# Kernel optimization log

Measured on AMD Instinct MI355X. Metric: run time of the kernel, lower is better.

## Reference

```python
import jax, jax.numpy as jnp
import numpy as np

N_FEATS = 400000
IN_CH = 64
OUT_CH = 64
KK = 9  # kH * kW for kernel_size=3


def setup_inputs() -> dict:
    key = jax.random.key(0)
    k1, k2, k3, k4 = jax.random.split(key, 4)
    in_feats = jax.random.normal(k1, (N_FEATS, IN_CH), dtype=jnp.float32)
    mask = jnp.ones((N_FEATS,), dtype=bool)
    adj_ids = jax.random.randint(k2, (N_FEATS, KK), 0, N_FEATS, dtype=jnp.int64)
    conv_weight = jax.random.normal(k3, (OUT_CH, KK * IN_CH), dtype=jnp.float32) * 0.02
    conv_bias = jax.random.normal(k4, (OUT_CH,), dtype=jnp.float32) * 0.02
    return {"in_feats": in_feats, "mask": mask, "adj_ids": adj_ids,
            "conv_weight": conv_weight, "conv_bias": conv_bias}


def reference(in_feats, mask, adj_ids, conv_weight, conv_bias):
    # Gather neighbor features: [num_conv_feats, kH*kW, in_channels]
    num_conv_feats = adj_ids.shape[0]
    gathered = in_feats[adj_ids]
    # Flatten kernel window and project: [num_conv_feats, out_channels]
    flat = gathered.reshape(num_conv_feats, -1)
    conv_out = jnp.einsum('nf,of->no', flat, conv_weight) + conv_bias
    # Scatter into masked rows: row i (where mask[i]) receives conv_out row
    # equal to its rank among True mask entries (matches out_feats[mask] = ...).
    pos = jnp.cumsum(mask.astype(jnp.int32)) - 1  # rank among True entries
    pos = jnp.clip(pos, 0, num_conv_feats - 1)
    out_feats = jnp.where(mask[:, None], conv_out[pos], jnp.float32(0))
    return out_feats
```

## Files before the change

kernel.cpp:

```cpp
#include <hip/hip_runtime.h>
#include <hip/hip_bf16.h>


#define KK 9
#define IN_CH 64
#define OUT_CH 64
#define KTOT 576
#define ROWS 16
#define NTILES 25000
#define ROW_BYTES 1152
#define TILE_BYTES 18432
#define NBLK 1024

typedef __attribute__((ext_vector_type(8))) short short8;
typedef __attribute__((ext_vector_type(4))) float f32x4;

__device__ __forceinline__ short bf1(float f) {
  __hip_bfloat16 h = __float2bfloat16(f);
  return *reinterpret_cast<short*>(&h);
}
__device__ __forceinline__ short8 pack8(float4 a, float4 b) {
  short8 v;
  v[0] = bf1(a.x); v[1] = bf1(a.y); v[2] = bf1(a.z); v[3] = bf1(a.w);
  v[4] = bf1(b.x); v[5] = bf1(b.y); v[6] = bf1(b.z); v[7] = bf1(b.w);
  return v;
}

__launch_bounds__(256)
__global__ void prepass_kernel(const float* __restrict__ feats,
                               unsigned short* __restrict__ fb) {
  const size_t idx = (size_t)blockIdx.x * 256 + threadIdx.x;
  const float* p = feats + idx * 8;
  float4 a = *(const float4*)p;
  float4 b = *(const float4*)(p + 4);
  *(short8*)(fb + idx * 8) = pack8(a, b);
}

template <bool PRE>
__launch_bounds__(256, 2)
__global__ void adjconv_kernel(const float* __restrict__ feats,
                               const unsigned short* __restrict__ fb,
                               const unsigned int* __restrict__ adj_raw,
                               const float* __restrict__ W,
                               const float* __restrict__ bias,
                               float* __restrict__ out) {
  __shared__ __align__(16) unsigned char lds[2 * TILE_BYTES];

  const int tid  = threadIdx.x;
  const int lane = tid & 63;
  const int wv   = tid >> 6;
  const int lrow = lane & 15;
  const int kg   = lane >> 4;
  const int bcol = (wv << 4) + lrow;

  bool is64 = true;
  #pragma unroll
  for (int j = 1; j < 16; j += 2) if (adj_raw[j] != 0u) is64 = false;
  const unsigned iscale = is64 ? 2u : 1u;

  short8 bfrag[18];
  #pragma unroll
  for (int ks = 0; ks < 18; ++ks) {
    const float* wp = W + bcol * KTOT + ks * 32 + kg * 8;
    bfrag[ks] = pack8(*(const float4*)wp, *(const float4*)(wp + 4));
  }
  const float bias_c = bias[bcol];

  short8 F[5];
  float4 G[5][2];
  unsigned idn[5];

  auto LOAD_IDS = [&](unsigned* ids, int wt_) {
    const size_t base = (size_t)wt_ * (ROWS * KK);
    #pragma unroll
    for (int i = 0; i < 5; ++i) {
      if (i < 4 || tid < 128) {
        const int cid = tid + (i << 8);
        const int row = cid / 72, ch = cid - row * 72;
        ids[i] = adj_raw[(base + row * KK + (ch >> 3)) * iscale];
      }
    }
  };
  auto GATHER = [&](const unsigned* ids) {
    #pragma unroll
    for (int i = 0; i < 5; ++i) {
      if (i < 4 || tid < 128) {
        const int cid = tid + (i << 8);
        const int row = cid / 72, ch = cid - row * 72;
        const int c8 = (ch & 7) << 3;
        if constexpr (PRE) {
          F[i] = *(const short8*)(fb + (size_t)ids[i] * IN_CH + c8);
        } else {
          const float* p = feats + (size_t)ids[i] * IN_CH + c8;
          G[i][0] = *(const float4*)p;
          G[i][1] = *(const float4*)(p + 4);
        }
      }
    }
  };
  auto WRITE = [&](unsigned char* buf) {
    #pragma unroll
    for (int i = 0; i < 5; ++i) {
      if (i < 4 || tid < 128) {
        const int cid = tid + (i << 8);
        const int row = cid / 72, ch = cid - row * 72;
        unsigned char* dst = buf + row * ROW_BYTES + ((ch ^ (row & 7)) << 4);
        if constexpr (PRE) *(short8*)dst = F[i];
        else               *(short8*)dst = pack8(G[i][0], G[i][1]);
      }
    }
  };

  int wt = blockIdx.x;
  {
    unsigned idc[5];
    LOAD_IDS(idc, wt);
    GATHER(idc);
    if (wt + NBLK < NTILES) LOAD_IDS(idn, wt + NBLK);
    WRITE(lds);
    __syncthreads();
  }

  int cur = 0;
  for (; wt < NTILES; wt += NBLK) {
    const bool hasn1 = (wt + NBLK) < NTILES;
    const bool hasn2 = (wt + 2 * NBLK) < NTILES;
    if (hasn1) GATHER(idn);
    if (hasn2) LOAD_IDS(idn, wt + 2 * NBLK);

    {
      const unsigned char* rbase = lds + cur * TILE_BYTES + lrow * ROW_BYTES;
      f32x4 acc = {0.f, 0.f, 0.f, 0.f};
      #pragma unroll
      for (int ks = 0; ks < 18; ++ks) {
        short8 a = *(const short8*)(rbase + ((((ks << 2) + kg) ^ (lrow & 7)) << 4));
        acc = __builtin_amdgcn_mfma_f32_16x16x32_bf16(a, bfrag[ks], acc, 0, 0, 0);
      }
      float* op = out + ((size_t)wt * ROWS + (kg << 2)) * OUT_CH + bcol;
      op[0 * OUT_CH] = acc[0] + bias_c;
      op[1 * OUT_CH] = acc[1] + bias_c;
      op[2 * OUT_CH] = acc[2] + bias_c;
      op[3 * OUT_CH] = acc[3] + bias_c;
    }

    if (hasn1) WRITE(lds + (cur ^ 1) * TILE_BYTES);
    __syncthreads();
    cur ^= 1;
  }
}

extern "C" void kernel_launch(void* const* d_in, const int* in_sizes, int n_in,
                              void* d_out, int out_size, void* d_ws, size_t ws_size,
                              hipStream_t stream) {
  const float* feats          = (const float*)d_in[0];
  const unsigned int* adj_raw = (const unsigned int*)d_in[2];
  const float* W              = (const float*)d_in[3];
  const float* bias           = (const float*)d_in[4];
  float* out                  = (float*)d_out;

  const size_t FB_BYTES = (size_t)400000 * 64 * 2;

  if (ws_size >= FB_BYTES) {
    unsigned short* fb = (unsigned short*)d_ws;
    hipLaunchKernelGGL(prepass_kernel, dim3(12500), dim3(256), 0, stream, feats, fb);
    hipLaunchKernelGGL((adjconv_kernel<true>), dim3(NBLK), dim3(256), 0, stream,
                       feats, fb, adj_raw, W, bias, out);
  } else {
    hipLaunchKernelGGL((adjconv_kernel<false>), dim3(NBLK), dim3(256), 0, stream,
                       feats, (const unsigned short*)nullptr, adj_raw, W, bias, out);
  }
}
```

Baseline: 123.9 us.

## Gather neighbor rows straight into LDS with global_load_lds and nontemporal I/O

In the bf16 precomputed path, the register-staged gather followed by ds_write is replaced with asynchronous global_load_lds copies of 16 bytes each, straight into the double-buffered LDS tile. The XOR swizzle moves from the LDS address onto the global source column chunk, so each row is stored contiguously while the MFMA reads stay conflict-free. The prepass now uses nontemporal loads and the output uses nontemporal stores. The aim is to cut VGPR pressure and VALU/LDS-write work in the gather stage. It depends on the compiler placing the right vmcnt waits before the barrier for the LDS-DMA writes.

```diff
diff --git a/kernel.cpp b/kernel.cpp
--- a/kernel.cpp
+++ b/kernel.cpp
@@ -14,29 +14,29 @@
 
 typedef __attribute__((ext_vector_type(8))) short short8;
 typedef __attribute__((ext_vector_type(4))) float f32x4;
+typedef float fv4 __attribute__((ext_vector_type(4)));
 
 __device__ __forceinline__ short bf1(float f) {
   __hip_bfloat16 h = __float2bfloat16(f);
   return *reinterpret_cast<short*>(&h);
 }
-__device__ __forceinline__ short8 pack8(float4 a, float4 b) {
+__device__ __forceinline__ short8 pack8(fv4 a, fv4 b) {
   short8 v;
-  v[0] = bf1(a.x); v[1] = bf1(a.y); v[2] = bf1(a.z); v[3] = bf1(a.w);
-  v[4] = bf1(b.x); v[5] = bf1(b.y); v[6] = bf1(b.z); v[7] = bf1(b.w);
+  v[0] = bf1(a[0]); v[1] = bf1(a[1]); v[2] = bf1(a[2]); v[3] = bf1(a[3]);
+  v[4] = bf1(b[0]); v[5] = bf1(b[1]); v[6] = bf1(b[2]); v[7] = bf1(b[3]);
   return v;
 }
 
 __launch_bounds__(256)
 __global__ void prepass_kernel(const float* __restrict__ feats,
                                unsigned short* __restrict__ fb) {
-  const size_t idx = (size_t)blockIdx.x * 256 + threadIdx.x;
-  const float* p = feats + idx * 8;
-  float4 a = *(const float4*)p;
-  float4 b = *(const float4*)(p + 4);
-  *(short8*)(fb + idx * 8) = pack8(a, b);
+  const size_t idx = ((size_t)blockIdx.x * 256 + threadIdx.x) * 8;
+  fv4 a = __builtin_nontemporal_load((const fv4*)(feats + idx));
+  fv4 b = __builtin_nontemporal_load((const fv4*)(feats + idx + 4));
+  *(short8*)(fb + idx) = pack8(a, b);
 }
 
-template <bool PRE>
+template <int MODE>
 __launch_bounds__(256, 2)
 __global__ void adjconv_kernel(const float* __restrict__ feats,
                                const unsigned short* __restrict__ fb,
@@ -62,13 +62,12 @@
   #pragma unroll
   for (int ks = 0; ks < 18; ++ks) {
     const float* wp = W + bcol * KTOT + ks * 32 + kg * 8;
-    bfrag[ks] = pack8(*(const float4*)wp, *(const float4*)(wp + 4));
+    bfrag[ks] = pack8(*(const fv4*)wp, *(const fv4*)(wp + 4));
   }
   const float bias_c = bias[bcol];
 
-  short8 F[5];
-  float4 G[5][2];
   unsigned idn[5];
+  fv4 G[5][2];
 
   auto LOAD_IDS = [&](unsigned* ids, int wt_) {
     const size_t base = (size_t)wt_ * (ROWS * KK);
@@ -76,37 +75,47 @@
     for (int i = 0; i < 5; ++i) {
       if (i < 4 || tid < 128) {
         const int cid = tid + (i << 8);
-        const int row = cid / 72, ch = cid - row * 72;
-        ids[i] = adj_raw[(base + row * KK + (ch >> 3)) * iscale];
+        const int row = cid / 72, chs = cid - row * 72;
+        ids[i] = adj_raw[(base + row * KK + (chs >> 3)) * iscale];
       }
     }
   };
-  auto GATHER = [&](const unsigned* ids) {
+
+  auto ISSUE = [&](unsigned char* buf, const unsigned* ids) {
     #pragma unroll
     for (int i = 0; i < 5; ++i) {
       if (i < 4 || tid < 128) {
         const int cid = tid + (i << 8);
-        const int row = cid / 72, ch = cid - row * 72;
-        const int c8 = (ch & 7) << 3;
-        if constexpr (PRE) {
-          F[i] = *(const short8*)(fb + (size_t)ids[i] * IN_CH + c8);
-        } else {
-          const float* p = feats + (size_t)ids[i] * IN_CH + c8;
-          G[i][0] = *(const float4*)p;
-          G[i][1] = *(const float4*)(p + 4);
-        }
+        const int row = cid / 72, chs = cid - row * 72;
+        const int cu = (chs & 7) ^ (row & 7);
+        const unsigned short* src = fb + (size_t)ids[i] * IN_CH + cu * 8;
+        __builtin_amdgcn_global_load_lds(
+            (const __attribute__((address_space(1))) unsigned int*)src,
+            (__attribute__((address_space(3))) unsigned int*)(buf + cid * 16),
+            16, 0, 0);
       }
     }
   };
-  auto WRITE = [&](unsigned char* buf) {
+
+  auto GATHER0 = [&](const unsigned* ids) {
     #pragma unroll
     for (int i = 0; i < 5; ++i) {
       if (i < 4 || tid < 128) {
         const int cid = tid + (i << 8);
-        const int row = cid / 72, ch = cid - row * 72;
-        unsigned char* dst = buf + row * ROW_BYTES + ((ch ^ (row & 7)) << 4);
-        if constexpr (PRE) *(short8*)dst = F[i];
-        else               *(short8*)dst = pack8(G[i][0], G[i][1]);
+        const int row = cid / 72, chs = cid - row * 72;
+        const float* p = feats + (size_t)ids[i] * IN_CH + ((chs & 7) << 3);
+        G[i][0] = *(const fv4*)p;
+        G[i][1] = *(const fv4*)(p + 4);
+      }
+    }
+  };
+  auto WRITE0 = [&](unsigned char* buf) {
+    #pragma unroll
+    for (int i = 0; i < 5; ++i) {
+      if (i < 4 || tid < 128) {
+        const int cid = tid + (i << 8);
+        const int row = cid / 72, chs = cid - row * 72;
+        *(short8*)(buf + row * ROW_BYTES + ((chs ^ (row & 7)) << 4)) = pack8(G[i][0], G[i][1]);
       }
     }
   };
@@ -115,9 +124,10 @@
   {
     unsigned idc[5];
     LOAD_IDS(idc, wt);
-    GATHER(idc);
+    if constexpr (MODE == 2) ISSUE(lds, idc);
+    else                     GATHER0(idc);
     if (wt + NBLK < NTILES) LOAD_IDS(idn, wt + NBLK);
-    WRITE(lds);
+    if constexpr (MODE == 0) WRITE0(lds);
     __syncthreads();
   }
 
@@ -125,7 +135,11 @@
   for (; wt < NTILES; wt += NBLK) {
     const bool hasn1 = (wt + NBLK) < NTILES;
     const bool hasn2 = (wt + 2 * NBLK) < NTILES;
-    if (hasn1) GATHER(idn);
+    if constexpr (MODE == 2) {
+      if (hasn1) ISSUE(lds + (cur ^ 1) * TILE_BYTES, idn);
+    } else {
+      if (hasn1) GATHER0(idn);
+    }
     if (hasn2) LOAD_IDS(idn, wt + 2 * NBLK);
 
     {
@@ -137,13 +151,15 @@
         acc = __builtin_amdgcn_mfma_f32_16x16x32_bf16(a, bfrag[ks], acc, 0, 0, 0);
       }
       float* op = out + ((size_t)wt * ROWS + (kg << 2)) * OUT_CH + bcol;
-      op[0 * OUT_CH] = acc[0] + bias_c;
-      op[1 * OUT_CH] = acc[1] + bias_c;
-      op[2 * OUT_CH] = acc[2] + bias_c;
-      op[3 * OUT_CH] = acc[3] + bias_c;
+      __builtin_nontemporal_store(acc[0] + bias_c, op);
+      __builtin_nontemporal_store(acc[1] + bias_c, op + OUT_CH);
+      __builtin_nontemporal_store(acc[2] + bias_c, op + 2 * OUT_CH);
+      __builtin_nontemporal_store(acc[3] + bias_c, op + 3 * OUT_CH);
     }
 
-    if (hasn1) WRITE(lds + (cur ^ 1) * TILE_BYTES);
+    if constexpr (MODE == 0) {
+      if (hasn1) WRITE0(lds + (cur ^ 1) * TILE_BYTES);
+    }
     __syncthreads();
     cur ^= 1;
   }
@@ -163,10 +179,10 @@
   if (ws_size >= FB_BYTES) {
     unsigned short* fb = (unsigned short*)d_ws;
     hipLaunchKernelGGL(prepass_kernel, dim3(12500), dim3(256), 0, stream, feats, fb);
-    hipLaunchKernelGGL((adjconv_kernel<true>), dim3(NBLK), dim3(256), 0, stream,
+    hipLaunchKernelGGL((adjconv_kernel<2>), dim3(NBLK), dim3(256), 0, stream,
                        feats, fb, adj_raw, W, bias, out);
   } else {
-    hipLaunchKernelGGL((adjconv_kernel<false>), dim3(NBLK), dim3(256), 0, stream,
+    hipLaunchKernelGGL((adjconv_kernel<0>), dim3(NBLK), dim3(256), 0, stream,
                        feats, (const unsigned short*)nullptr, adj_raw, W, bias, out);
   }
 }
```

Result: slower. 126.9 us (+2.4%).

## Warp-specialize adjconv into producer/consumer waves with 4-slot LDS ring

Applied to the files above, without the earlier changes.

Splits each 512-thread block into four producer waves and four consumer waves. Producers gather neighbor rows straight into a 4-slot LDS ring using global_load_lds, and consumers run the MFMA projection. The two sides hand off slots through LDS counter flags polled with s_sleep instead of block-wide barriers, which lets several tiles' gathers stay in flight and overlap with compute. The prepass also switches to nontemporal loads. This adds spin-wait overhead and the risk of ordering bugs in the flag protocol. The grid is halved to 512 blocks and each block needs 73KB of LDS, which may limit occupancy.

```diff
diff --git a/kernel.cpp b/kernel.cpp
--- a/kernel.cpp
+++ b/kernel.cpp
@@ -9,143 +9,171 @@
 #define ROWS 16
 #define NTILES 25000
 #define ROW_BYTES 1152
-#define TILE_BYTES 18432
-#define NBLK 1024
+#define SLOT_BYTES 18432
+#define NSLOT 4
+#define NBLK 512
+#define LDS_BYTES (NSLOT * SLOT_BYTES + 32)
 
 typedef __attribute__((ext_vector_type(8))) short short8;
 typedef __attribute__((ext_vector_type(4))) float f32x4;
+typedef float fv4 __attribute__((ext_vector_type(4)));
 
 __device__ __forceinline__ short bf1(float f) {
   __hip_bfloat16 h = __float2bfloat16(f);
   return *reinterpret_cast<short*>(&h);
 }
-__device__ __forceinline__ short8 pack8(float4 a, float4 b) {
+__device__ __forceinline__ short8 pack8(fv4 a, fv4 b) {
   short8 v;
-  v[0] = bf1(a.x); v[1] = bf1(a.y); v[2] = bf1(a.z); v[3] = bf1(a.w);
-  v[4] = bf1(b.x); v[5] = bf1(b.y); v[6] = bf1(b.z); v[7] = bf1(b.w);
+  v[0] = bf1(a[0]); v[1] = bf1(a[1]); v[2] = bf1(a[2]); v[3] = bf1(a[3]);
+  v[4] = bf1(b[0]); v[5] = bf1(b[1]); v[6] = bf1(b[2]); v[7] = bf1(b[3]);
   return v;
 }
 
 __launch_bounds__(256)
 __global__ void prepass_kernel(const float* __restrict__ feats,
                                unsigned short* __restrict__ fb) {
-  const size_t idx = (size_t)blockIdx.x * 256 + threadIdx.x;
-  const float* p = feats + idx * 8;
-  float4 a = *(const float4*)p;
-  float4 b = *(const float4*)(p + 4);
-  *(short8*)(fb + idx * 8) = pack8(a, b);
-}
-
-template <bool PRE>
-__launch_bounds__(256, 2)
+  const size_t idx = ((size_t)blockIdx.x * 256 + threadIdx.x) * 8;
+  fv4 a = __builtin_nontemporal_load((const fv4*)(feats + idx));
+  fv4 b = __builtin_nontemporal_load((const fv4*)(feats + idx + 4));
+  *(short8*)(fb + idx) = pack8(a, b);
+}
+
+template <int PRE>
+__launch_bounds__(512, 2)
 __global__ void adjconv_kernel(const float* __restrict__ feats,
                                const unsigned short* __restrict__ fb,
                                const unsigned int* __restrict__ adj_raw,
                                const float* __restrict__ W,
                                const float* __restrict__ bias,
                                float* __restrict__ out) {
-  __shared__ __align__(16) unsigned char lds[2 * TILE_BYTES];
+  extern __shared__ __align__(16) unsigned char lds[];
+  int* flags = (int*)(lds + NSLOT * SLOT_BYTES);
+  volatile int* vflags = flags;
 
   const int tid  = threadIdx.x;
   const int lane = tid & 63;
   const int wv   = tid >> 6;
-  const int lrow = lane & 15;
-  const int kg   = lane >> 4;
-  const int bcol = (wv << 4) + lrow;
+  if (tid < 8) flags[tid] = 0;
+  __syncthreads();
 
   bool is64 = true;
   #pragma unroll
   for (int j = 1; j < 16; j += 2) if (adj_raw[j] != 0u) is64 = false;
   const unsigned iscale = is64 ? 2u : 1u;
 
-  short8 bfrag[18];
-  #pragma unroll
-  for (int ks = 0; ks < 18; ++ks) {
-    const float* wp = W + bcol * KTOT + ks * 32 + kg * 8;
-    bfrag[ks] = pack8(*(const float4*)wp, *(const float4*)(wp + 4));
-  }
-  const float bias_c = bias[bcol];
-
-  short8 F[5];
-  float4 G[5][2];
-  unsigned idn[5];
-
-  auto LOAD_IDS = [&](unsigned* ids, int wt_) {
-    const size_t base = (size_t)wt_ * (ROWS * KK);
+  const int bid = blockIdx.x;
+  const int T = (NTILES - 1 - bid) / NBLK + 1;
+
+  if (wv < 4) {
+    const int p = tid;
+    unsigned idn[5];
+    fv4 G[5][2];
+
+#define P_FOREACH(body)                                                      \
+    _Pragma("unroll")                                                        \
+    for (int i = 0; i < 5; ++i) {                                            \
+      if (i < 4 || p < 128) {                                                \
+        const int cid = p + (i << 8);                                        \
+        const int row = cid / 72, chs = cid - row * 72;                      \
+        body                                                                 \
+      }                                                                      \
+    }
+
+#define LOAD_IDS(t_) {                                                       \
+    const int tc = ((t_) < T) ? (t_) : (T - 1);                              \
+    const size_t base = (size_t)(bid + (size_t)tc * NBLK) * (ROWS * KK);     \
+    P_FOREACH( idn[i] = adj_raw[(base + row * KK + (chs >> 3)) * iscale]; )  \
+  }
+
+#define ISSUE(slot_) {                                                       \
+    unsigned char* buf = lds + (slot_) * SLOT_BYTES;                         \
+    P_FOREACH(                                                               \
+      const int cu = (chs & 7) ^ (row & 7);                                  \
+      const unsigned short* src = fb + (size_t)idn[i] * IN_CH + cu * 8;      \
+      __builtin_amdgcn_global_load_lds(                                      \
+          (const __attribute__((address_space(1))) unsigned int*)src,        \
+          (__attribute__((address_space(3))) unsigned int*)(buf + cid * 16), \
+          16, 0, 0); )                                                       \
+  }
+
+#define GATHER0() P_FOREACH(                                                 \
+      const float* q = feats + (size_t)idn[i] * IN_CH + ((chs & 7) << 3);    \
+      G[i][0] = *(const fv4*)q; G[i][1] = *(const fv4*)(q + 4); )
+
+#define WRITE0(slot_) {                                                      \
+    unsigned char* buf = lds + (slot_) * SLOT_BYTES;                         \
+    P_FOREACH( *(short8*)(buf + row * ROW_BYTES + ((chs ^ (row & 7)) << 4))  \
+                   = pack8(G[i][0], G[i][1]); )                              \
+  }
+
+    LOAD_IDS(0);
+    asm volatile("s_waitcnt vmcnt(0)" ::: "memory");
+    if constexpr (PRE) { ISSUE(0); }
+    else               { GATHER0(); }
+    LOAD_IDS(1);
+
+    for (int t = 0; t < T; ++t) {
+      const int s = t & 3;
+      if (t + 1 < T) {
+        const int s1 = (t + 1) & 3;
+        const int tgt = 4 * ((t + 1) >> 2);
+        while (vflags[4 + s1] < tgt) __builtin_amdgcn_s_sleep(2);
+        __builtin_amdgcn_sched_barrier(0);
+      }
+      asm volatile("s_waitcnt vmcnt(0)" ::: "memory");
+      if constexpr (!PRE) {
+        WRITE0(s);
+        asm volatile("s_waitcnt lgkmcnt(0)" ::: "memory");
+      }
+      __builtin_amdgcn_sched_barrier(0);
+      if (lane == 0) atomicAdd(&flags[s], 1);
+      if (t + 1 < T) {
+        if constexpr (PRE) { ISSUE((t + 1) & 3); }
+        else               { GATHER0(); }
+        LOAD_IDS(t + 2);
+      }
+    }
+#undef P_FOREACH
+#undef LOAD_IDS
+#undef ISSUE
+#undef GATHER0
+#undef WRITE0
+  } else {
+    const int cb   = wv - 4;
+    const int lrow = lane & 15;
+    const int kg   = lane >> 4;
+    const int bcol = (cb << 4) + lrow;
+
+    short8 bfrag[18];
     #pragma unroll
-    for (int i = 0; i < 5; ++i) {
-      if (i < 4 || tid < 128) {
-        const int cid = tid + (i << 8);
-        const int row = cid / 72, ch = cid - row * 72;
-        ids[i] = adj_raw[(base + row * KK + (ch >> 3)) * iscale];
-      }
-    }
-  };
-  auto GATHER = [&](const unsigned* ids) {
-    #pragma unroll
-    for (int i = 0; i < 5; ++i) {
-      if (i < 4 || tid < 128) {
-        const int cid = tid + (i << 8);
-        const int row = cid / 72, ch = cid - row * 72;
-        const int c8 = (ch & 7) << 3;
-        if constexpr (PRE) {
-          F[i] = *(const short8*)(fb + (size_t)ids[i] * IN_CH + c8);
-        } else {
-          const float* p = feats + (size_t)ids[i] * IN_CH + c8;
-          G[i][0] = *(const float4*)p;
-          G[i][1] = *(const float4*)(p + 4);
-        }
-      }
-    }
-  };
-  auto WRITE = [&](unsigned char* buf) {
-    #pragma unroll
-    for (int i = 0; i < 5; ++i) {
-      if (i < 4 || tid < 128) {
-        const int cid = tid + (i << 8);
-        const int row = cid / 72, ch = cid - row * 72;
-        unsigned char* dst = buf + row * ROW_BYTES + ((ch ^ (row & 7)) << 4);
-        if constexpr (PRE) *(short8*)dst = F[i];
-        else               *(short8*)dst = pack8(G[i][0], G[i][1]);
-      }
-    }
-  };
-
-  int wt = blockIdx.x;
-  {
-    unsigned idc[5];
-    LOAD_IDS(idc, wt);
-    GATHER(idc);
-    if (wt + NBLK < NTILES) LOAD_IDS(idn, wt + NBLK);
-    WRITE(lds);
-    __syncthreads();
-  }
-
-  int cur = 0;
-  for (; wt < NTILES; wt += NBLK) {
-    const bool hasn1 = (wt + NBLK) < NTILES;
-    const bool hasn2 = (wt + 2 * NBLK) < NTILES;
-    if (hasn1) GATHER(idn);
-    if (hasn2) LOAD_IDS(idn, wt + 2 * NBLK);
-
-    {
-      const unsigned char* rbase = lds + cur * TILE_BYTES + lrow * ROW_BYTES;
+    for (int ks = 0; ks < 18; ++ks) {
+      const float* wp = W + bcol * KTOT + ks * 32 + kg * 8;
+      bfrag[ks] = pack8(*(const fv4*)wp, *(const fv4*)(wp + 4));
+    }
+    const float bias_c = bias[bcol];
+
+    for (int t = 0; t < T; ++t) {
+      const int s = t & 3;
+      const int tgt = 4 * ((t >> 2) + 1);
+      while (vflags[s] < tgt) __builtin_amdgcn_s_sleep(2);
+      __builtin_amdgcn_sched_barrier(0);
+
+      const unsigned char* rbase = lds + s * SLOT_BYTES + lrow * ROW_BYTES;
       f32x4 acc = {0.f, 0.f, 0.f, 0.f};
       #pragma unroll
       for (int ks = 0; ks < 18; ++ks) {
         short8 a = *(const short8*)(rbase + ((((ks << 2) + kg) ^ (lrow & 7)) << 4));
         acc = __builtin_amdgcn_mfma_f32_16x16x32_bf16(a, bfrag[ks], acc, 0, 0, 0);
       }
-      float* op = out + ((size_t)wt * ROWS + (kg << 2)) * OUT_CH + bcol;
+      float* op = out + (((size_t)bid + (size_t)t * NBLK) * ROWS + (kg << 2)) * OUT_CH + bcol;
       op[0 * OUT_CH] = acc[0] + bias_c;
       op[1 * OUT_CH] = acc[1] + bias_c;
       op[2 * OUT_CH] = acc[2] + bias_c;
       op[3 * OUT_CH] = acc[3] + bias_c;
-    }
-
-    if (hasn1) WRITE(lds + (cur ^ 1) * TILE_BYTES);
-    __syncthreads();
-    cur ^= 1;
+
+      __builtin_amdgcn_sched_barrier(0);
+      if (lane == 0) atomicAdd(&flags[4 + s], 1);
+    }
   }
 }
 
@@ -162,11 +190,15 @@
 
   if (ws_size >= FB_BYTES) {
     unsigned short* fb = (unsigned short*)d_ws;
+    (void)hipFuncSetAttribute((const void*)(adjconv_kernel<1>),
+                              hipFuncAttributeMaxDynamicSharedMemorySize, LDS_BYTES);
     hipLaunchKernelGGL(prepass_kernel, dim3(12500), dim3(256), 0, stream, feats, fb);
-    hipLaunchKernelGGL((adjconv_kernel<true>), dim3(NBLK), dim3(256), 0, stream,
+    hipLaunchKernelGGL((adjconv_kernel<1>), dim3(NBLK), dim3(512), LDS_BYTES, stream,
                        feats, fb, adj_raw, W, bias, out);
   } else {
-    hipLaunchKernelGGL((adjconv_kernel<false>), dim3(NBLK), dim3(256), 0, stream,
+    (void)hipFuncSetAttribute((const void*)(adjconv_kernel<0>),
+                              hipFuncAttributeMaxDynamicSharedMemorySize, LDS_BYTES);
+    hipLaunchKernelGGL((adjconv_kernel<0>), dim3(NBLK), dim3(512), LDS_BYTES, stream,
                        feats, (const unsigned short*)nullptr, adj_raw, W, bias, out);
   }
 }
```

Measured after the change: 119.2 us. 1.04x faster.
